# Kernel optimization log

Measured on AMD Instinct MI355X. Metric: run time of the kernel, lower is better.

Reference implementation:

```python
import jax, jax.numpy as jnp
import numpy as np
from jax import lax

B, S, C, D, V = 256, 50, 40, 256, 20000
T_DIFF = 1000
BETA_START, BETA_END = 1e-4, 2e-2


def _lstm(x, Wih, Whh, bih, bhh):
    # x: [B,S,D]; single-layer LSTM, batch_first, eval mode (no dropout)
    Bb = x.shape[0]
    H = Whh.shape[1]
    def step(carry, xt):
        h, c = carry
        g = xt @ Wih.T + bih + h @ Whh.T + bhh  # [B,4H]
        i, f, gg, o = jnp.split(g, 4, axis=-1)
        i = jax.nn.sigmoid(i); f = jax.nn.sigmoid(f)
        gg = jnp.tanh(gg); o = jax.nn.sigmoid(o)
        c = f * c + i * gg
        h = o * jnp.tanh(c)
        return (h, c), h
    h0 = jnp.zeros((Bb, H), x.dtype)
    (_, _), hs = lax.scan(step, (h0, h0), x.transpose(1, 0, 2))
    return hs.transpose(1, 0, 2)  # [B,S,H]


def setup_inputs() -> dict:
    key = jax.random.key(0)
    ks = jax.random.split(key, 20)
    sc = 0.05
    inp = {
        'input_seqs': jax.random.randint(ks[0], (B, S, C), 0, V),
        'masks': jnp.zeros((B, S), jnp.int32),
        'lengths': jax.random.randint(ks[1], (B,), 1, S + 1),
        'seq_time_step': jax.random.uniform(ks[2], (B, S), jnp.float32),
        'code_masks': jnp.zeros((B, S, C), jnp.int32),
        'diffusion_time_t': jax.random.randint(ks[3], (B,), 0, T_DIFF),
        'normal_noise': jax.random.normal(ks[4], (B, S, D), jnp.float32),
        # learned parameters
        'emb': jax.random.normal(ks[5], (V + 1, D), jnp.float32) * sc,
        'Wih': jax.random.normal(ks[6], (4 * D, D), jnp.float32) * sc,
        'Whh': jax.random.normal(ks[7], (4 * D, D), jnp.float32) * sc,
        'bih': jnp.zeros((4 * D,), jnp.float32),
        'bhh': jnp.zeros((4 * D,), jnp.float32),
        'Whk': jax.random.normal(ks[8], (D, D), jnp.float32) * sc,
        'bhk': jnp.zeros((D,), jnp.float32),
        'W1': jax.random.normal(ks[9], (64, 2 * D), jnp.float32) * sc,
        'b1': jnp.zeros((64,), jnp.float32),
        'W2': jax.random.normal(ks[10], (2, 64), jnp.float32) * sc,
        'b2': jnp.zeros((2,), jnp.float32),
        'Wdiff': jax.random.normal(ks[11], (D, D), jnp.float32) * sc,
        'bdiff': jnp.zeros((D,), jnp.float32),
        'temb': jax.random.normal(ks[12], (T_DIFF, D), jnp.float32) * sc,
        'Wout': jax.random.normal(ks[13], (2, D), jnp.float32) * sc,
        'bout': jnp.zeros((2,), jnp.float32),
    }
    # padding_idx row zeroed like nn.Embedding(padding_idx=-1)
    inp['emb'] = inp['emb'].at[V].set(0.0)
    return inp


def reference(input_seqs, masks, lengths, seq_time_step, code_masks,
              diffusion_time_t, normal_noise,
              emb, Wih, Whh, bih, bhh, Whk, bhk, W1, b1, W2, b2,
              Wdiff, bdiff, temb, Wout, bout):
    # embedding sum over codes per visit
    x = emb[input_seqs].sum(axis=2)  # [B,S,D]
    rnn_out = _lstm(x, Wih, Whh, bih, bhh)  # [B,S,D]

    # vectorized alignment loop: e_k is ALWAYS x[:,0] (as in source),
    # position i>=1 attends between e_k and w_hk(rnn_out[i-1])
    w = rnn_out @ Whk.T + bhk  # [B,S,D]
    e_k = x[:, :1, :]  # [B,1,D]
    wprev = w[:, :-1, :]  # [B,S-1,D] -> timestep i uses w[i-1]
    cat = jnp.concatenate([jnp.broadcast_to(e_k, wprev.shape), wprev], -1)
    attn = jax.nn.softmax(jnp.tanh(cat @ W1.T + b1) @ W2.T + b2, axis=-1)  # [B,S-1,2]
    aligned_rest = e_k * attn[..., 0:1] + wprev * attn[..., 1:2]
    aligned_e_t = jnp.concatenate([e_k, aligned_rest], axis=1)  # [B,S,D]

    # diffusion noising (linear beta schedule as in ehr.yml defaults)
    betas = jnp.linspace(BETA_START, BETA_END, T_DIFF, dtype=jnp.float32)
    alpha = jnp.cumprod(1.0 - betas)[diffusion_time_t][:, None, None]
    noisy = aligned_e_t * jnp.sqrt(alpha) + normal_noise * jnp.sqrt(1.0 - alpha)

    # UNet surrogate (source unavailable): timestep-conditioned linear map
    predicted_noise = (noisy + temb[diffusion_time_t][:, None, :]) @ Wdiff + bdiff

    gen_x = aligned_e_t + (normal_noise - predicted_noise)
    pool_x = jnp.max(x, axis=1) @ Wout.T + bout  # [B,2]
    gen_pool_x = jnp.max(gen_x, axis=1) @ Wout.T + bout  # [B,2]
    return (pool_x, gen_pool_x, predicted_noise, normal_noise)
```

## Files before the change

### kernel.cpp

```cpp
#include <hip/hip_runtime.h>
#include <cmath>

#define Bb 256
#define Ss 50
#define Cc 40
#define Dd 256
#define Vv 20000

typedef __bf16 bf16;
typedef __bf16 bf16x8 __attribute__((ext_vector_type(8)));
typedef float f32x4 __attribute__((ext_vector_type(4)));
typedef unsigned long long u64;

#define GL2LDS(g, l) __builtin_amdgcn_global_load_lds( \
    (__attribute__((address_space(1))) void*)(g), \
    (__attribute__((address_space(3))) void*)(l), 16, 0, 0)

#define OFFB_GATES    0ull
#define OFFB_ALIGNED  0ull
#define OFFB_WBB      13107200ull
#define OFFB_TMPB     25952256ull
#define OFFB_H1       32505856ull
#define OFFB_X        52428800ull
#define OFFB_XB       65536000ull
#define OFFB_RNNB     72089600ull
#define OFFB_W        78643200ull
#define OFFB_BAR      91750400ull
#define OFFB_WIHB     92012544ull
#define OFFB_WHHB     92536832ull
#define OFFB_WHKB     93061120ull
#define OFFB_W1B      93192192ull
#define OFFB_WDTB     93257728ull
#define OFFB_SALPHA   93388800ull
#define OFFB_SBETA    93389824ull

template<int BM, int BN, int ACT>
__global__ __launch_bounds__(256) void mfma_gemm(
    const bf16* __restrict__ A, int lda,
    const bf16* __restrict__ B, int ldb,
    const float* __restrict__ bias1, const float* __restrict__ bias2,
    float* __restrict__ C, bf16* __restrict__ Cb, int ldc, int K)
{
    constexpr int BK = 32;
    constexpr int NF = BN / 32;
    __shared__ bf16 As[BM * BK];
    __shared__ bf16 Bs[BN * BK];
    const int tid  = threadIdx.x;
    const int wave = tid >> 6;
    const int lane = tid & 63;
    const int m0 = blockIdx.x * BM;
    const int n0 = blockIdx.y * BN;
    const int wm = (wave >> 1) * 64;
    const int wn = (wave & 1) * (BN / 2);

    f32x4 acc[4][NF];
#pragma unroll
    for (int i = 0; i < 4; ++i)
#pragma unroll
        for (int j = 0; j < NF; ++j) acc[i][j] = (f32x4){0.f, 0.f, 0.f, 0.f};

    const int ar = tid >> 2;
    const int ac = tid & 3;
    const int sw = ac ^ (ar & 3);
    const int lr = lane & 15;
    const int q  = lane >> 4;

    for (int k0 = 0; k0 < K; k0 += BK) {
        __syncthreads();
#pragma unroll
        for (int it = 0; it < BM / 64; ++it) {
            const bf16* gp = A + (size_t)(m0 + it * 64 + ar) * lda + k0 + sw * 8;
            GL2LDS(gp, As + it * 2048 + wave * 512);
        }
#pragma unroll
        for (int it = 0; it < BN / 64; ++it) {
            const bf16* gp = B + (size_t)(n0 + it * 64 + ar) * ldb + k0 + sw * 8;
            GL2LDS(gp, Bs + it * 2048 + wave * 512);
        }
        __syncthreads();

        bf16x8 af[4], bfv[NF];
#pragma unroll
        for (int fm = 0; fm < 4; ++fm) {
            int m = wm + fm * 16 + lr;
            af[fm] = *(const bf16x8*)(As + m * 32 + ((q ^ (m & 3)) * 8));
        }
#pragma unroll
        for (int fn = 0; fn < NF; ++fn) {
            int n = wn + fn * 16 + lr;
            bfv[fn] = *(const bf16x8*)(Bs + n * 32 + ((q ^ (n & 3)) * 8));
        }
#pragma unroll
        for (int fm = 0; fm < 4; ++fm)
#pragma unroll
            for (int fn = 0; fn < NF; ++fn)
                acc[fm][fn] = __builtin_amdgcn_mfma_f32_16x16x32_bf16(
                    af[fm], bfv[fn], acc[fm][fn], 0, 0, 0);
    }

    const int rbase = q * 4;
#pragma unroll
    for (int fn = 0; fn < NF; ++fn) {
        const int col = n0 + wn + fn * 16 + lr;
        float bb = 0.f;
        if (bias1) bb += bias1[col];
        if (bias2) bb += bias2[col];
#pragma unroll
        for (int fm = 0; fm < 4; ++fm) {
            f32x4 v = acc[fm][fn];
#pragma unroll
            for (int r = 0; r < 4; ++r) {
                const int row = m0 + wm + fm * 16 + rbase + r;
                float val = v[r] + bb;
                if (ACT == 1) val = tanhf(val);
                C[(size_t)row * ldc + col] = val;
                if (Cb) Cb[(size_t)row * ldc + col] = (bf16)val;
            }
        }
    }
}

__global__ __launch_bounds__(256) void h1_gemm(
    const bf16* __restrict__ xb, const bf16* __restrict__ wbb,
    const bf16* __restrict__ W1b,
    const float* __restrict__ b1, float* __restrict__ H1)
{
    constexpr int BM = 128, BN = 64, BK = 32, NF = 2;
    constexpr int K = 512;
    __shared__ bf16 As[BM * BK];
    __shared__ bf16 Bs[BN * BK];
    const int tid  = threadIdx.x;
    const int wave = tid >> 6;
    const int lane = tid & 63;
    const int m0 = blockIdx.x * BM;
    const int wm = (wave >> 1) * 64;
    const int wn = (wave & 1) * 32;

    f32x4 acc[4][NF];
#pragma unroll
    for (int i = 0; i < 4; ++i)
#pragma unroll
        for (int j = 0; j < NF; ++j) acc[i][j] = (f32x4){0.f, 0.f, 0.f, 0.f};

    const int ar = tid >> 2;
    const int ac = tid & 3;
    const int sw = ac ^ (ar & 3);
    const int lr = lane & 15;
    const int q  = lane >> 4;

    for (int k0 = 0; k0 < K; k0 += BK) {
        __syncthreads();
#pragma unroll
        for (int it = 0; it < 2; ++it) {
            const int row = m0 + it * 64 + ar;
            const int b = row / (Ss - 1), t = row - b * (Ss - 1);
            const int col = k0 + sw * 8;
            const bf16* gp = (col < 256)
                ? xb  + (size_t)b * (Ss * Dd) + col
                : wbb + ((size_t)(b * Ss + t)) * Dd + (col - 256);
            GL2LDS(gp, As + it * 2048 + wave * 512);
        }
        {
            const bf16* gp = W1b + (size_t)ar * K + k0 + sw * 8;
            GL2LDS(gp, Bs + wave * 512);
        }
        __syncthreads();

        bf16x8 af[4], bfv[NF];
#pragma unroll
        for (int fm = 0; fm < 4; ++fm) {
            int m = wm + fm * 16 + lr;
            af[fm] = *(const bf16x8*)(As + m * 32 + ((q ^ (m & 3)) * 8));
        }
#pragma unroll
        for (int fn = 0; fn < NF; ++fn) {
            int n = wn + fn * 16 + lr;
            bfv[fn] = *(const bf16x8*)(Bs + n * 32 + ((q ^ (n & 3)) * 8));
        }
#pragma unroll
        for (int fm = 0; fm < 4; ++fm)
#pragma unroll
            for (int fn = 0; fn < NF; ++fn)
                acc[fm][fn] = __builtin_amdgcn_mfma_f32_16x16x32_bf16(
                    af[fm], bfv[fn], acc[fm][fn], 0, 0, 0);
    }

    const int rbase = q * 4;
#pragma unroll
    for (int fn = 0; fn < NF; ++fn) {
        const int col = wn + fn * 16 + lr;
        const float bb = b1[col];
#pragma unroll
        for (int fm = 0; fm < 4; ++fm) {
            f32x4 v = acc[fm][fn];
#pragma unroll
            for (int r = 0; r < 4; ++r) {
                const int row = m0 + wm + fm * 16 + rbase + r;
                H1[(size_t)row * 64 + col] = tanhf(v[r] + bb);
            }
        }
    }
}

__global__ __launch_bounds__(512, 2) void lstm_quad(
    const bf16* __restrict__ Whhb,
    const float* __restrict__ gates,
    bf16* __restrict__ rnnb,
    unsigned* __restrict__ bar,
    const float* __restrict__ xf,
    const float* __restrict__ Wout, const float* __restrict__ bout,
    float* __restrict__ outp)
{
    if (blockIdx.x >= 64) {
        __shared__ float r0[4], r1[4];
        const int b = blockIdx.x - 64;
        const int tid = threadIdx.x;
        if (tid < 256) {
            float m = -INFINITY;
            for (int s = 0; s < Ss; ++s)
                m = fmaxf(m, xf[((size_t)b * Ss + s) * Dd + tid]);
            float v0 = m * Wout[tid];
            float v1 = m * Wout[Dd + tid];
#pragma unroll
            for (int off = 32; off; off >>= 1) {
                v0 += __shfl_down(v0, off);
                v1 += __shfl_down(v1, off);
            }
            if ((tid & 63) == 0) { r0[tid >> 6] = v0; r1[tid >> 6] = v1; }
        }
        __syncthreads();
        if (tid == 0) {
            outp[b * 2 + 0] = r0[0] + r0[1] + r0[2] + r0[3] + bout[0];
            outp[b * 2 + 1] = r1[0] + r1[1] + r1[2] + r1[3] + bout[1];
        }
        return;
    }

    __shared__ bf16 hb0[16 * 256];
    __shared__ bf16 hb1[16 * 256];
    __shared__ float pacc[4][4][16][17];
    const int tid  = threadIdx.x;
    const int w    = tid >> 6;
    const int lane = tid & 63;
    const int lr   = lane & 15;
    const int q    = lane >> 4;
    const int bm   = blockIdx.x & 15;
    const int bd   = blockIdx.x >> 4;
    const int kh   = w >> 2;
    const int ct   = w & 3;
    const int dg   = bd * 64 + ct * 16 + lr;

    f32x4 wfr[4][4];
#pragma unroll
    for (int g = 0; g < 4; ++g) {
        const bf16* brow = Whhb + (size_t)(g * 256 + dg) * Dd + kh * 128 + q * 8;
#pragma unroll
        for (int kc = 0; kc < 4; ++kc)
            wfr[g][kc] = *(const f32x4*)(brow + kc * 32);
    }

    const float* gp[4];
#pragma unroll
    for (int r = 0; r < 4; ++r)
        gp[r] = gates + (size_t)(bm * 16 + q * 4 + r) * (Ss * 1024) + dg;

    const int xrow = tid >> 4, xc8 = tid & 15;
    const size_t my_base = ((size_t)(bm * 16 + xrow) * Ss) * Dd + bd * 64 + xc8 * 4;
    const int pack_off = xrow * 512 + (((bd * 8 + (xc8 >> 1)) ^ (xrow & 7)) << 4) + (xc8 & 1) * 8;

    const int pA  = tid >> 8;
    const int pdA = pA + (pA >= bd ? 1 : 0);
    const int pdB = 2 + (2 >= bd ? 1 : 0);
    const int rowA = (tid >> 4) & 15, xqA = tid & 15;
    const size_t gA = ((size_t)(bm * 16 + rowA) * Ss) * Dd + pdA * 64 + xqA * 4;
    const size_t gB = ((size_t)(bm * 16 + xrow) * Ss) * Dd + pdB * 64 + xc8 * 4;
    const int unpA = rowA * 512 + (((pdA * 8 + (xqA >> 1)) ^ (rowA & 7)) << 4) + (xqA & 1) * 8;
    const int unpB = xrow * 512 + (((pdB * 8 + (xc8 >> 1)) ^ (xrow & 7)) << 4) + (xc8 & 1) * 8;
    unsigned* myf = bar + (bm * 4 + bd) * 32;
    unsigned* pfA = bar + (bm * 4 + pdA) * 32;
    unsigned* pfB = bar + (bm * 4 + pdB) * 32;

    int ew_off[4];
#pragma unroll
    for (int r = 0; r < 4; ++r) {
        const int row = q * 4 + r;
        ew_off[r] = row * 512 + (((dg >> 3) ^ (row & 7)) << 4) + (dg & 7) * 2;
    }

    float c[4] = {0.f, 0.f, 0.f, 0.f};
    float gaA[4][4], gaB[4][4];
    if (kh == 0) {
#pragma unroll
        for (int r = 0; r < 4; ++r)
#pragma unroll
            for (int g = 0; g < 4; ++g) gaA[g][r] = gp[r][g * 256];
    }

#define STEP(T, GACUR, GANEXT, RD, WR, FIRST)                                   \
    {                                                                           \
        f32x4 acc[4];                                                           \
        _Pragma("unroll")                                                       \
        for (int g = 0; g < 4; ++g) acc[g] = (f32x4){0.f, 0.f, 0.f, 0.f};       \
        if (!(FIRST)) {                                                         \
            bf16x8 af[4];                                                       \
            _Pragma("unroll")                                                   \
            for (int kc = 0; kc < 4; ++kc)                                      \
                af[kc] = *(const bf16x8*)((const char*)(RD) + lr * 512          \
                         + (((kh * 16 + kc * 4 + q) ^ (lr & 7)) << 4));         \
            _Pragma("unroll")                                                   \
            for (int kc = 0; kc < 4; ++kc)                                      \
                _Pragma("unroll")                                               \
                for (int g = 0; g < 4; ++g)                                     \
                    acc[g] = __builtin_amdgcn_mfma_f32_16x16x32_bf16(           \
                        af[kc], __builtin_bit_cast(bf16x8, wfr[g][kc]),         \
                        acc[g], 0, 0, 0);                                       \
        }                                                                       \
        if (kh == 1) {                                                          \
            _Pragma("unroll")                                                   \
            for (int g = 0; g < 4; ++g)                                         \
                _Pragma("unroll")                                               \
                for (int r = 0; r < 4; ++r)                                     \
                    pacc[ct][g][q * 4 + r][lr] = acc[g][r];                     \
        }                                                                       \
        __syncthreads();                          \
        if (kh == 0) {                                                          \
            _Pragma("unroll")                                                   \
            for (int r = 0; r < 4; ++r) {                                       \
                float gi = acc[0][r] + pacc[ct][0][q * 4 + r][lr] + GACUR[0][r];\
                float gf = acc[1][r] + pacc[ct][1][q * 4 + r][lr] + GACUR[1][r];\
                float gg = acc[2][r] + pacc[ct][2][q * 4 + r][lr] + GACUR[2][r];\
                float go = acc[3][r] + pacc[ct][3][q * 4 + r][lr] + GACUR[3][r];\
                float ii  = 1.f / (1.f + expf(-gi));                            \
                float ff  = 1.f / (1.f + expf(-gf));                            \
                float g2t = tanhf(gg);                                          \
                float oo  = 1.f / (1.f + expf(-go));                            \
                c[r] = ff * c[r] + ii * g2t;                                    \
                *(bf16*)((char*)(WR) + ew_off[r]) = (bf16)(oo * tanhf(c[r]));   \
            }                                                                   \
        }                                                                       \
        __syncthreads();                          \
        if (tid < 256) {                                                        \
            u64 v = *(const u64*)((const char*)(WR) + pack_off);                \
            __hip_atomic_store((u64*)(rnnb + my_base + (size_t)(T) * Dd), v,    \
                               __ATOMIC_RELAXED, __HIP_MEMORY_SCOPE_AGENT);     \
        }                                                                       \
        if ((T) != Ss - 1) {                                                    \
            __syncthreads();        \
            if (tid == 0)                                                       \
                __hip_atomic_store(myf, (unsigned)((T) + 1),                    \
                                   __ATOMIC_RELAXED, __HIP_MEMORY_SCOPE_AGENT); \
            if (kh == 0) {            \
                _Pragma("unroll")                                               \
                for (int r = 0; r < 4; ++r)                                     \
                    _Pragma("unroll")                                           \
                    for (int g = 0; g < 4; ++g)                                 \
                        GANEXT[g][r] = gp[r][(size_t)((T) + 1) * 1024 + g * 256];\
            }                                                                   \
            while (__hip_atomic_load(pfA, __ATOMIC_RELAXED,                     \
                                     __HIP_MEMORY_SCOPE_AGENT)                  \
                   < (unsigned)((T) + 1)) {}                                    \
            {                                                                   \
                u64 rv = __hip_atomic_load(                                     \
                    (const u64*)(rnnb + gA + (size_t)(T) * Dd),                 \
                    __ATOMIC_RELAXED, __HIP_MEMORY_SCOPE_AGENT);                \
                *(u64*)((char*)(WR) + unpA) = rv;                               \
            }                                                                   \
            if (tid < 256) {                                                    \
                while (__hip_atomic_load(pfB, __ATOMIC_RELAXED,                 \
                                         __HIP_MEMORY_SCOPE_AGENT)              \
                       < (unsigned)((T) + 1)) {}                                \
                u64 rv = __hip_atomic_load(                                     \
                    (const u64*)(rnnb + gB + (size_t)(T) * Dd),                 \
                    __ATOMIC_RELAXED, __HIP_MEMORY_SCOPE_AGENT);                \
                *(u64*)((char*)(WR) + unpB) = rv;                               \
            }                                                                   \
            __syncthreads();           \
        }                                                                       \
    }

    for (int t2 = 0; t2 < Ss; t2 += 2) {
        STEP(t2,     gaA, gaB, hb1, hb0, (t2 == 0));
        STEP(t2 + 1, gaB, gaA, hb0, hb1, false);
    }
#undef STEP
}

__global__ __launch_bounds__(256) void prep_kernel(
    const float* __restrict__ Wih, bf16* __restrict__ Wihb,
    const float* __restrict__ Whh, bf16* __restrict__ Whhb,
    const float* __restrict__ Whk, bf16* __restrict__ Whkb,
    const float* __restrict__ W1,  bf16* __restrict__ W1b,
    const float* __restrict__ Wdiff, bf16* __restrict__ WdTb,
    const int* __restrict__ tdiff, float* __restrict__ salpha,
    float* __restrict__ sbeta, unsigned* __restrict__ bar)
{
    __shared__ float t[32][33];
    int bx = blockIdx.x;
    const int tid = threadIdx.x;
    if (bx < 1024) { int i = bx * 256 + tid; Wihb[i] = (bf16)Wih[i]; return; }
    bx -= 1024;
    if (bx < 1024) { int i = bx * 256 + tid; Whhb[i] = (bf16)Whh[i]; return; }
    bx -= 1024;
    if (bx < 256)  { int i = bx * 256 + tid; Whkb[i] = (bf16)Whk[i]; return; }
    bx -= 256;
    if (bx < 128)  { int i = bx * 256 + tid; W1b[i]  = (bf16)W1[i];  return; }
    bx -= 128;
    if (bx < 64) {
        const int c0 = (bx & 7) * 32, r0 = (bx >> 3) * 32;
        const int tx = tid & 31, ty = tid >> 5;
        for (int i = ty; i < 32; i += 8)
            t[i][tx] = Wdiff[(size_t)(r0 + i) * 256 + c0 + tx];
        __syncthreads();
        for (int i = ty; i < 32; i += 8)
            WdTb[(size_t)(c0 + i) * 256 + r0 + tx] = (bf16)t[tx][i];
        return;
    }
#pragma unroll
    for (int j = 0; j < 8; ++j) bar[tid * 8 + j] = 0u;
    const int tt = tdiff[tid];
    const float step = (0.02f - 1e-4f) / 999.f;
    float prod = 1.f;
    for (int j = 0; j <= tt; ++j) prod *= (1.f - (1e-4f + j * step));
    salpha[tid] = sqrtf(prod);
    sbeta[tid]  = sqrtf(fmaxf(1.f - prod, 0.f));
}

__global__ __launch_bounds__(256) void embed_kernel(
    const int* __restrict__ seqs, const float* __restrict__ emb,
    float* __restrict__ x, bf16* __restrict__ xb)
{
    __shared__ int idx[4][Cc];
    const int tid = threadIdx.x;
    const int w = tid >> 6, l = tid & 63;
    const int bs0 = blockIdx.x * 4;
    if (tid < 4 * Cc) idx[tid / Cc][tid % Cc] = seqs[(size_t)bs0 * Cc + tid];
    __syncthreads();
    f32x4 s = (f32x4){0.f, 0.f, 0.f, 0.f};
#pragma unroll 8
    for (int c = 0; c < Cc; ++c)
        s += *(const f32x4*)(emb + (size_t)idx[w][c] * Dd + l * 4);
    const size_t o = (size_t)(bs0 + w) * Dd + l * 4;
    *(f32x4*)(x + o) = s;
    bf16 b4[4] = {(bf16)s[0], (bf16)s[1], (bf16)s[2], (bf16)s[3]};
    *(u64*)(xb + o) = *(const u64*)b4;
}

__global__ __launch_bounds__(256) void attn_diff_kernel(
    const float* __restrict__ x, const float* __restrict__ w,
    const float* __restrict__ H1, const float* __restrict__ W2,
    const float* __restrict__ b2, const float* __restrict__ noise,
    const float* __restrict__ temb, const int* __restrict__ tdiff,
    const float* __restrict__ salpha, const float* __restrict__ sbeta,
    float* __restrict__ aligned, bf16* __restrict__ tmpb,
    float* __restrict__ noise_out)
{
    __shared__ float sa[2];
    const int bs = blockIdx.x;
    const int b = bs / Ss, s = bs % Ss;
    const int d = threadIdx.x;
    if (s > 0 && threadIdx.x < 64) {
        const int r = b * (Ss - 1) + (s - 1);
        const int j = threadIdx.x;
        float h = H1[(size_t)r * 64 + j];
        float v0 = h * W2[j];
        float v1 = h * W2[64 + j];
#pragma unroll
        for (int off = 32; off; off >>= 1) { v0 += __shfl_down(v0, off); v1 += __shfl_down(v1, off); }
        if (j == 0) {
            float z0 = v0 + b2[0], z1 = v1 + b2[1];
            float m = fmaxf(z0, z1);
            float e0 = expf(z0 - m), e1 = expf(z1 - m);
            float inv = 1.f / (e0 + e1);
            sa[0] = e0 * inv;
            sa[1] = e1 * inv;
        }
    }
    __syncthreads();
    const float ek = x[((size_t)b * Ss) * Dd + d];
    float v;
    if (s == 0) {
        v = ek;
    } else {
        v = ek * sa[0] + w[((size_t)b * Ss + s - 1) * Dd + d] * sa[1];
    }
    const size_t i = (size_t)bs * Dd + d;
    aligned[i] = v;
    const int t = tdiff[b];
    tmpb[i] = (bf16)(v * salpha[b] + noise[i] * sbeta[b] + temb[(size_t)t * Dd + d]);
    noise_out[i] = noise[i];
}

__global__ __launch_bounds__(256) void gen_pool_kernel(
    const float* __restrict__ aligned, const float* __restrict__ noise,
    const float* __restrict__ pred, const float* __restrict__ Wout,
    const float* __restrict__ bout, float* __restrict__ outp)
{
    __shared__ float r0[4], r1[4];
    const int b = blockIdx.x, d = threadIdx.x;
    float m = -INFINITY;
    for (int s = 0; s < Ss; ++s) {
        const size_t i = ((size_t)b * Ss + s) * Dd + d;
        m = fmaxf(m, aligned[i] + noise[i] - pred[i]);
    }
    float v0 = m * Wout[d];
    float v1 = m * Wout[Dd + d];
#pragma unroll
    for (int off = 32; off; off >>= 1) { v0 += __shfl_down(v0, off); v1 += __shfl_down(v1, off); }
    const int lane = d & 63, wv = d >> 6;
    if (lane == 0) { r0[wv] = v0; r1[wv] = v1; }
    __syncthreads();
    if (d == 0) {
        outp[b * 2 + 0] = r0[0] + r0[1] + r0[2] + r0[3] + bout[0];
        outp[b * 2 + 1] = r1[0] + r1[1] + r1[2] + r1[3] + bout[1];
    }
}

extern "C" void kernel_launch(void* const* d_in, const int* in_sizes, int n_in,
                              void* d_out, int out_size, void* d_ws, size_t ws_size,
                              hipStream_t stream)
{
    const int*   seqs  = (const int*)d_in[0];
    const int*   tdiff = (const int*)d_in[5];
    const float* noise = (const float*)d_in[6];
    const float* emb   = (const float*)d_in[7];
    const float* Wih   = (const float*)d_in[8];
    const float* Whh   = (const float*)d_in[9];
    const float* bih   = (const float*)d_in[10];
    const float* bhh   = (const float*)d_in[11];
    const float* Whk   = (const float*)d_in[12];
    const float* bhk   = (const float*)d_in[13];
    const float* W1    = (const float*)d_in[14];
    const float* b1    = (const float*)d_in[15];
    const float* W2    = (const float*)d_in[16];
    const float* b2    = (const float*)d_in[17];
    const float* Wdiff = (const float*)d_in[18];
    const float* bdiff = (const float*)d_in[19];
    const float* temb  = (const float*)d_in[20];
    const float* Wout  = (const float*)d_in[21];
    const float* bout  = (const float*)d_in[22];

    float* outp = (float*)d_out;
    char*  wsb  = (char*)d_ws;

    float* gates   = (float*)(wsb + OFFB_GATES);
    float* aligned = (float*)(wsb + OFFB_ALIGNED);
    bf16*  wbb     = (bf16*) (wsb + OFFB_WBB);
    bf16*  tmpb    = (bf16*) (wsb + OFFB_TMPB);
    float* H1      = (float*)(wsb + OFFB_H1);
    float* x       = (float*)(wsb + OFFB_X);
    bf16*  xb      = (bf16*) (wsb + OFFB_XB);
    bf16*  rnnb    = (bf16*) (wsb + OFFB_RNNB);
    float* wbuf    = (float*)(wsb + OFFB_W);
    unsigned* bar  = (unsigned*)(wsb + OFFB_BAR);
    bf16*  Wihb    = (bf16*) (wsb + OFFB_WIHB);
    bf16*  Whhb    = (bf16*) (wsb + OFFB_WHHB);
    bf16*  Whkb    = (bf16*) (wsb + OFFB_WHKB);
    bf16*  W1b     = (bf16*) (wsb + OFFB_W1B);
    bf16*  WdTb    = (bf16*) (wsb + OFFB_WDTB);
    float* salpha  = (float*)(wsb + OFFB_SALPHA);
    float* sbeta   = (float*)(wsb + OFFB_SBETA);

    float* pred_out  = outp + 1024;
    float* noise_out = outp + 1024 + (size_t)Bb * Ss * Dd;

    prep_kernel<<<2497, 256, 0, stream>>>(Wih, Wihb, Whh, Whhb, Whk, Whkb,
                                          W1, W1b, Wdiff, WdTb,
                                          tdiff, salpha, sbeta, bar);

    embed_kernel<<<(Bb * Ss) / 4, 256, 0, stream>>>(seqs, emb, x, xb);

    mfma_gemm<128, 128, 0><<<dim3(100, 8), 256, 0, stream>>>(
        xb, 256, Wihb, 256, bih, bhh, gates, nullptr, 1024, 256);

    lstm_quad<<<64 + Bb, 512, 0, stream>>>(Whhb, gates, rnnb, bar,
                                           x, Wout, bout, outp);

    mfma_gemm<128, 128, 0><<<dim3(100, 2), 256, 0, stream>>>(
        rnnb, 256, Whkb, 256, bhk, nullptr, wbuf, wbb, 256, 256);

    h1_gemm<<<dim3(98, 1), 256, 0, stream>>>(xb, wbb, W1b, b1, H1);

    attn_diff_kernel<<<Bb * Ss, 256, 0, stream>>>(
        x, wbuf, H1, W2, b2, noise, temb, tdiff, salpha, sbeta,
        aligned, tmpb, noise_out);

    mfma_gemm<128, 128, 0><<<dim3(100, 2), 256, 0, stream>>>(
        tmpb, 256, WdTb, 256, bdiff, nullptr, pred_out, nullptr, 256, 256);

    gen_pool_kernel<<<Bb, 256, 0, stream>>>(aligned, noise, pred_out, Wout, bout, outp + 512);
}
```

Baseline: 470.8 us.

## Fuse attention, diffusion GEMM and gen-pool into one per-batch tail kernel

Merges embed into the prep kernel launch, and replaces the attn_diff, Wdiff GEMM and gen_pool kernels with one per-batch tail kernel. That kernel keeps aligned and noisy activations in LDS, runs the 50x256x256 MFMA GEMM on them with rows padded to 64, and does the max-pool reduction in the epilogue. This removes the global round trips for aligned and tmpb and drops two kernel launches. In exchange the tail runs on only 256 blocks, wastes MFMA work on the padding rows, and uses a large LDS footprint per block.

```diff
diff --git a/kernel.cpp b/kernel.cpp
--- a/kernel.cpp
+++ b/kernel.cpp
@@ -17,9 +17,7 @@
     (__attribute__((address_space(3))) void*)(l), 16, 0, 0)
 
 #define OFFB_GATES    0ull
-#define OFFB_ALIGNED  0ull
 #define OFFB_WBB      13107200ull
-#define OFFB_TMPB     25952256ull
 #define OFFB_H1       32505856ull
 #define OFFB_X        52428800ull
 #define OFFB_XB       65536000ull
@@ -392,9 +390,12 @@
     const float* __restrict__ W1,  bf16* __restrict__ W1b,
     const float* __restrict__ Wdiff, bf16* __restrict__ WdTb,
     const int* __restrict__ tdiff, float* __restrict__ salpha,
-    float* __restrict__ sbeta, unsigned* __restrict__ bar)
+    float* __restrict__ sbeta, unsigned* __restrict__ bar,
+    const int* __restrict__ seqs, const float* __restrict__ emb,
+    float* __restrict__ x, bf16* __restrict__ xb)
 {
     __shared__ float t[32][33];
+    __shared__ int idx[4][Cc];
     int bx = blockIdx.x;
     const int tid = threadIdx.x;
     if (bx < 1024) { int i = bx * 256 + tid; Wihb[i] = (bf16)Wih[i]; return; }
@@ -415,24 +416,21 @@
             WdTb[(size_t)(c0 + i) * 256 + r0 + tx] = (bf16)t[tx][i];
         return;
     }
-#pragma unroll
-    for (int j = 0; j < 8; ++j) bar[tid * 8 + j] = 0u;
-    const int tt = tdiff[tid];
-    const float step = (0.02f - 1e-4f) / 999.f;
-    float prod = 1.f;
-    for (int j = 0; j <= tt; ++j) prod *= (1.f - (1e-4f + j * step));
-    salpha[tid] = sqrtf(prod);
-    sbeta[tid]  = sqrtf(fmaxf(1.f - prod, 0.f));
-}
-
-__global__ __launch_bounds__(256) void embed_kernel(
-    const int* __restrict__ seqs, const float* __restrict__ emb,
-    float* __restrict__ x, bf16* __restrict__ xb)
-{
-    __shared__ int idx[4][Cc];
-    const int tid = threadIdx.x;
+    bx -= 64;
+    if (bx == 0) {
+#pragma unroll
+        for (int j = 0; j < 8; ++j) bar[tid * 8 + j] = 0u;
+        const int tt = tdiff[tid];
+        const float step = (0.02f - 1e-4f) / 999.f;
+        float prod = 1.f;
+        for (int j = 0; j <= tt; ++j) prod *= (1.f - (1e-4f + j * step));
+        salpha[tid] = sqrtf(prod);
+        sbeta[tid]  = sqrtf(fmaxf(1.f - prod, 0.f));
+        return;
+    }
+    bx -= 1;
     const int w = tid >> 6, l = tid & 63;
-    const int bs0 = blockIdx.x * 4;
+    const int bs0 = bx * 4;
     if (tid < 4 * Cc) idx[tid / Cc][tid % Cc] = seqs[(size_t)bs0 * Cc + tid];
     __syncthreads();
     f32x4 s = (f32x4){0.f, 0.f, 0.f, 0.f};
@@ -445,73 +443,141 @@
     *(u64*)(xb + o) = *(const u64*)b4;
 }
 
-__global__ __launch_bounds__(256) void attn_diff_kernel(
-    const float* __restrict__ x, const float* __restrict__ w,
+__global__ __launch_bounds__(256) void tail_kernel(
+    const float* __restrict__ x, const float* __restrict__ wbuf,
     const float* __restrict__ H1, const float* __restrict__ W2,
     const float* __restrict__ b2, const float* __restrict__ noise,
     const float* __restrict__ temb, const int* __restrict__ tdiff,
     const float* __restrict__ salpha, const float* __restrict__ sbeta,
-    float* __restrict__ aligned, bf16* __restrict__ tmpb,
-    float* __restrict__ noise_out)
+    const bf16* __restrict__ WdTb, const float* __restrict__ bdiff,
+    const float* __restrict__ Wout, const float* __restrict__ bout,
+    float* __restrict__ pred_out, float* __restrict__ noise_out,
+    float* __restrict__ outp_gen)
 {
-    __shared__ float sa[2];
-    const int bs = blockIdx.x;
-    const int b = bs / Ss, s = bs % Ss;
-    const int d = threadIdx.x;
-    if (s > 0 && threadIdx.x < 64) {
-        const int r = b * (Ss - 1) + (s - 1);
-        const int j = threadIdx.x;
-        float h = H1[(size_t)r * 64 + j];
-        float v0 = h * W2[j];
-        float v1 = h * W2[64 + j];
+    __shared__ float alignedL[Ss * 256];
+    __shared__ bf16  tmpbL[64 * 256];
+    __shared__ bf16  Bs[256 * 32];
+    __shared__ float saL[Ss - 1][2];
+    __shared__ float rr0[4], rr1[4];
+
+    const int b    = blockIdx.x;
+    const int tid  = threadIdx.x;
+    const int wave = tid >> 6;
+    const int lane = tid & 63;
+    const int lr   = lane & 15;
+    const int q    = lane >> 4;
+
+    for (int t = wave; t < Ss - 1; t += 4) {
+        const int r = b * (Ss - 1) + t;
+        float h = H1[(size_t)r * 64 + lane];
+        float v0 = h * W2[lane];
+        float v1 = h * W2[64 + lane];
 #pragma unroll
         for (int off = 32; off; off >>= 1) { v0 += __shfl_down(v0, off); v1 += __shfl_down(v1, off); }
-        if (j == 0) {
+        if (lane == 0) {
             float z0 = v0 + b2[0], z1 = v1 + b2[1];
             float m = fmaxf(z0, z1);
             float e0 = expf(z0 - m), e1 = expf(z1 - m);
             float inv = 1.f / (e0 + e1);
-            sa[0] = e0 * inv;
-            sa[1] = e1 * inv;
+            saL[t][0] = e0 * inv;
+            saL[t][1] = e1 * inv;
         }
     }
     __syncthreads();
-    const float ek = x[((size_t)b * Ss) * Dd + d];
-    float v;
-    if (s == 0) {
-        v = ek;
-    } else {
-        v = ek * sa[0] + w[((size_t)b * Ss + s - 1) * Dd + d] * sa[1];
-    }
-    const size_t i = (size_t)bs * Dd + d;
-    aligned[i] = v;
-    const int t = tdiff[b];
-    tmpb[i] = (bf16)(v * salpha[b] + noise[i] * sbeta[b] + temb[(size_t)t * Dd + d]);
-    noise_out[i] = noise[i];
-}
-
-__global__ __launch_bounds__(256) void gen_pool_kernel(
-    const float* __restrict__ aligned, const float* __restrict__ noise,
-    const float* __restrict__ pred, const float* __restrict__ Wout,
-    const float* __restrict__ bout, float* __restrict__ outp)
-{
-    __shared__ float r0[4], r1[4];
-    const int b = blockIdx.x, d = threadIdx.x;
-    float m = -INFINITY;
-    for (int s = 0; s < Ss; ++s) {
-        const size_t i = ((size_t)b * Ss + s) * Dd + d;
-        m = fmaxf(m, aligned[i] + noise[i] - pred[i]);
-    }
-    float v0 = m * Wout[d];
-    float v1 = m * Wout[Dd + d];
+
+    {
+        const int d = tid;
+        const float ek = x[((size_t)b * Ss) * Dd + d];
+        const int tt = tdiff[b];
+        const float sa_ = salpha[b], sb_ = sbeta[b];
+        const float te = temb[(size_t)tt * Dd + d];
+        for (int s = 0; s < Ss; ++s) {
+            float v;
+            if (s == 0) v = ek;
+            else v = ek * saL[s - 1][0]
+                   + wbuf[((size_t)b * Ss + s - 1) * Dd + d] * saL[s - 1][1];
+            alignedL[s * 256 + d] = v;
+            const size_t i = ((size_t)b * Ss + s) * Dd + d;
+            const float nz = noise[i];
+            noise_out[i] = nz;
+            const int off = s * 512 + (((d >> 3) ^ (s & 7)) << 4) + (d & 7) * 2;
+            *(bf16*)((char*)tmpbL + off) = (bf16)(v * sa_ + nz * sb_ + te);
+        }
+#pragma unroll
+        for (int s = Ss; s < 64; ++s) {
+            const int off = s * 512 + (((d >> 3) ^ (s & 7)) << 4) + (d & 7) * 2;
+            *(bf16*)((char*)tmpbL + off) = (bf16)0.f;
+        }
+    }
+
+    f32x4 acc[4][4];
+#pragma unroll
+    for (int i = 0; i < 4; ++i)
+#pragma unroll
+        for (int j = 0; j < 4; ++j) acc[i][j] = (f32x4){0.f, 0.f, 0.f, 0.f};
+
+    const int ar = tid >> 2, ac = tid & 3, sw = ac ^ (ar & 3);
+    const int wn = wave * 64;
+
+    for (int k0 = 0; k0 < 256; k0 += 32) {
+        __syncthreads();
+#pragma unroll
+        for (int it = 0; it < 4; ++it) {
+            const bf16* gp2 = WdTb + (size_t)(it * 64 + ar) * 256 + k0 + sw * 8;
+            GL2LDS(gp2, Bs + it * 2048 + wave * 512);
+        }
+        __syncthreads();
+        bf16x8 af[4], bfv[4];
+#pragma unroll
+        for (int fm = 0; fm < 4; ++fm) {
+            const int m = fm * 16 + lr;
+            af[fm] = *(const bf16x8*)((const char*)tmpbL + m * 512
+                      + ((((k0 >> 3) + q) ^ (m & 7)) << 4));
+        }
+#pragma unroll
+        for (int fn = 0; fn < 4; ++fn) {
+            const int n = wn + fn * 16 + lr;
+            bfv[fn] = *(const bf16x8*)(Bs + n * 32 + ((q ^ (n & 3)) * 8));
+        }
+#pragma unroll
+        for (int fm = 0; fm < 4; ++fm)
+#pragma unroll
+            for (int fn = 0; fn < 4; ++fn)
+                acc[fm][fn] = __builtin_amdgcn_mfma_f32_16x16x32_bf16(
+                    af[fm], bfv[fn], acc[fm][fn], 0, 0, 0);
+    }
+
+    float v0 = 0.f, v1 = 0.f;
+#pragma unroll
+    for (int fn = 0; fn < 4; ++fn) {
+        const int col = wn + fn * 16 + lr;
+        const float bd_ = bdiff[col];
+        float mx = -INFINITY;
+#pragma unroll
+        for (int fm = 0; fm < 4; ++fm) {
+#pragma unroll
+            for (int r = 0; r < 4; ++r) {
+                const int row = fm * 16 + q * 4 + r;
+                if (row < Ss) {
+                    const float pred = acc[fm][fn][r] + bd_;
+                    const size_t i = ((size_t)b * Ss + row) * Dd + col;
+                    pred_out[i] = pred;
+                    const float gen = alignedL[row * 256 + col] + noise[i] - pred;
+                    mx = fmaxf(mx, gen);
+                }
+            }
+        }
+        mx = fmaxf(mx, __shfl_xor(mx, 16));
+        mx = fmaxf(mx, __shfl_xor(mx, 32));
+        if (q == 0) { v0 += mx * Wout[col]; v1 += mx * Wout[Dd + col]; }
+    }
 #pragma unroll
     for (int off = 32; off; off >>= 1) { v0 += __shfl_down(v0, off); v1 += __shfl_down(v1, off); }
-    const int lane = d & 63, wv = d >> 6;
-    if (lane == 0) { r0[wv] = v0; r1[wv] = v1; }
+    if (lane == 0) { rr0[wave] = v0; rr1[wave] = v1; }
     __syncthreads();
-    if (d == 0) {
-        outp[b * 2 + 0] = r0[0] + r0[1] + r0[2] + r0[3] + bout[0];
-        outp[b * 2 + 1] = r1[0] + r1[1] + r1[2] + r1[3] + bout[1];
+    if (tid == 0) {
+        outp_gen[b * 2 + 0] = rr0[0] + rr0[1] + rr0[2] + rr0[3] + bout[0];
+        outp_gen[b * 2 + 1] = rr1[0] + rr1[1] + rr1[2] + rr1[3] + bout[1];
     }
 }
 
@@ -543,9 +609,7 @@
     char*  wsb  = (char*)d_ws;
 
     float* gates   = (float*)(wsb + OFFB_GATES);
-    float* aligned = (float*)(wsb + OFFB_ALIGNED);
     bf16*  wbb     = (bf16*) (wsb + OFFB_WBB);
-    bf16*  tmpb    = (bf16*) (wsb + OFFB_TMPB);
     float* H1      = (float*)(wsb + OFFB_H1);
     float* x       = (float*)(wsb + OFFB_X);
     bf16*  xb      = (bf16*) (wsb + OFFB_XB);
@@ -563,11 +627,10 @@
     float* pred_out  = outp + 1024;
     float* noise_out = outp + 1024 + (size_t)Bb * Ss * Dd;
 
-    prep_kernel<<<2497, 256, 0, stream>>>(Wih, Wihb, Whh, Whhb, Whk, Whkb,
+    prep_kernel<<<5697, 256, 0, stream>>>(Wih, Wihb, Whh, Whhb, Whk, Whkb,
                                           W1, W1b, Wdiff, WdTb,
-                                          tdiff, salpha, sbeta, bar);
-
-    embed_kernel<<<(Bb * Ss) / 4, 256, 0, stream>>>(seqs, emb, x, xb);
+                                          tdiff, salpha, sbeta, bar,
+                                          seqs, emb, x, xb);
 
     mfma_gemm<128, 128, 0><<<dim3(100, 8), 256, 0, stream>>>(
         xb, 256, Wihb, 256, bih, bhh, gates, nullptr, 1024, 256);
@@ -580,12 +643,7 @@
 
     h1_gemm<<<dim3(98, 1), 256, 0, stream>>>(xb, wbb, W1b, b1, H1);
 
-    attn_diff_kernel<<<Bb * Ss, 256, 0, stream>>>(
+    tail_kernel<<<Bb, 256, 0, stream>>>(
         x, wbuf, H1, W2, b2, noise, temb, tdiff, salpha, sbeta,
-        aligned, tmpb, noise_out);
-
-    mfma_gemm<128, 128, 0><<<dim3(100, 2), 256, 0, stream>>>(
-        tmpb, 256, WdTb, 256, bdiff, nullptr, pred_out, nullptr, 256, 256);
-
-    gen_pool_kernel<<<Bb, 256, 0, stream>>>(aligned, noise, pred_out, Wout, bout, outp + 512);
+        WdTb, bdiff, Wout, bout, pred_out, noise_out, outp + 512);
 }
```

After: 423.4 us. -10.1%, faster.
